# Kernel tuning notes

Measured on AMD Instinct MI355X. Metric: run time of the kernel, lower is better.

Reference implementation:

```python
import jax, jax.numpy as jnp
import numpy as np

B, D, L, K = 4096, 2048, 16384, 64  # batch, input_dim, latent_dim, topk


def setup_inputs() -> dict:
    key = jax.random.key(0)
    k_x, k_w = jax.random.split(key, 2)
    x = jax.random.normal(k_x, (B, D), dtype=jnp.float32)
    # torch init: randn(input_dim, latent_dim) / sqrt(input_dim)
    W_enc = jax.random.normal(k_w, (D, L), dtype=jnp.float32) / np.float32(np.sqrt(D))
    b_enc = jnp.zeros((L,), dtype=jnp.float32)
    b_dec = jnp.zeros((D,), dtype=jnp.float32)
    return {"x": x, "W_enc": W_enc, "b_enc": b_enc, "b_dec": b_dec, "k": K}


def reference(x, W_enc, b_enc, b_dec, k):
    # encode: [B, D] @ [D, L] + [L]
    z = x @ W_enc + b_enc
    # topk sparsify on |z| (do_abs_topk=True): scatter a 0/1 mask, multiply
    _, idx = jax.lax.top_k(jnp.abs(z), k)                      # idx: [B, k]
    rows = jnp.arange(z.shape[0])[:, None]                     # [B, 1]
    mask = jnp.zeros_like(z).at[rows, idx].set(1.0)            # [B, L]
    z_sparse = z * mask
    # decode with tied weights: [B, L] @ [L, D] + [D]
    recon = z_sparse @ W_enc.T + b_dec
    return recon, z_sparse
```

## Files before the change

kernel.cpp:

```cpp
#include <hip/hip_runtime.h>
#include <stdint.h>

#define NB 4096
#define DD 2048
#define LL 16384
#define KT 64
#define WCAP 24
#define TAU 1.2e-2f
#define T3 1e-4f

typedef unsigned short u16;
typedef __bf16 bf16x8 __attribute__((ext_vector_type(8)));
typedef float f32x4 __attribute__((ext_vector_type(4)));
typedef unsigned short u16x4 __attribute__((ext_vector_type(4)));
typedef unsigned short u16x8 __attribute__((ext_vector_type(8)));

__device__ __forceinline__ float bf2f(u16 b) {
  return __uint_as_float(((unsigned)b) << 16);
}
__device__ __forceinline__ u16 f2bf(float f) {
  unsigned u = __float_as_uint(f);
  unsigned r = u + 0x7fffu + ((u >> 16) & 1u);
  return (u16)(r >> 16);
}

__global__ __launch_bounds__(256) void prep_x(const float* __restrict__ X,
                                              u16* __restrict__ Xh) {
  int i = (blockIdx.x * 256 + threadIdx.x) * 4;
  float4 v = *(const float4*)(X + i);
  u16x4 h;
  h[0] = f2bf(v.x); h[1] = f2bf(v.y); h[2] = f2bf(v.z); h[3] = f2bf(v.w);
  *(u16x4*)(Xh + i) = h;
}

__global__ __launch_bounds__(256) void prep_w(const float* __restrict__ W,
                                              u16* __restrict__ Wh,
                                              u16* __restrict__ Wl,
                                              float* __restrict__ Wt) {
  __shared__ float tile[64][65];
  int l0 = blockIdx.x * 64, d0 = blockIdx.y * 64;
  int t = threadIdx.x;
  int lx = (t & 15) * 4;
  int dq = t >> 4;
#pragma unroll
  for (int p = 0; p < 4; ++p) {
    int d = dq + p * 16;
    float4 v = *(const float4*)(W + (size_t)(d0 + d) * LL + l0 + lx);
    tile[d][lx + 0] = v.x; tile[d][lx + 1] = v.y;
    tile[d][lx + 2] = v.z; tile[d][lx + 3] = v.w;
  }
  __syncthreads();
  int dx = (t & 15) * 4;
  int lq = t >> 4;
#pragma unroll
  for (int p = 0; p < 4; ++p) {
    int l = lq + p * 16;
    u16x4 h, lo;
    float4 wv;
#pragma unroll
    for (int q = 0; q < 4; ++q) {
      float w = tile[dx + q][l];
      u16 hb = f2bf(w);
      h[q] = hb;
      lo[q] = f2bf(w - bf2f(hb));
      ((float*)&wv)[q] = w;
    }
    size_t o = (size_t)(l0 + l) * DD + d0 + dx;
    *(u16x4*)(Wh + o) = h;
    *(u16x4*)(Wl + o) = lo;
    *(float4*)(Wt + o) = wv;
  }
}

#define TBM 256
#define TBN 256
#define TBK 64
#define NKT (DD / TBK)

__device__ __forceinline__ void async16(const u16* g, u16* l) {
  __builtin_amdgcn_global_load_lds(
      (const __attribute__((address_space(1))) unsigned int*)g,
      (__attribute__((address_space(3))) unsigned int*)l, 16, 0, 0);
}

#define STAGE(HF, TAU_)                                                      \
  do {                                                                       \
    const u16* g_ = ((HF) < 2 ? Abase : Bbase) +                             \
                    (size_t)(((HF)&1) * 128 + rr) * DD + ((TAU_) << 6) +     \
                    scol;                                                    \
    u16* l_ = ((HF) < 2 ? As : Bs) + ((TAU_)&1) * (TBM * TBK) +              \
              (((HF)&1) * 128) * TBK + t * 8;                                \
    async16(g_, l_);                                                         \
    async16(g_ + (size_t)64 * DD, l_ + 4096);                                \
  } while (0)

#define LDA(DST, DB, MQ)                                                     \
  do {                                                                       \
    const u16* p_ = As + (DB) * (TBM * TBK) + (wm + (MQ)*64 + fr) * TBK;     \
    _Pragma("unroll") for (int i_ = 0; i_ < 4; ++i_) {                       \
      DST[i_][0] = *(const bf16x8*)(p_ + i_ * (16 * TBK) + c0);              \
      DST[i_][1] = *(const bf16x8*)(p_ + i_ * (16 * TBK) + c1);              \
    }                                                                        \
  } while (0)

#define LDBQ(DB, NQ)                                                         \
  do {                                                                       \
    const u16* p_ = Bs + (DB) * (TBN * TBK) + (wn + (NQ)*32 + fr) * TBK;     \
    _Pragma("unroll") for (int j_ = 0; j_ < 2; ++j_) {                       \
      bq[j_][0] = *(const bf16x8*)(p_ + j_ * (16 * TBK) + c0);               \
      bq[j_][1] = *(const bf16x8*)(p_ + j_ * (16 * TBK) + c1);               \
    }                                                                        \
  } while (0)

#define MFMAQ_R(AF, MQ, NQ, IB, IE)                                          \
  do {                                                                       \
    _Pragma("unroll") for (int i_ = (IB); i_ < (IE); ++i_)                   \
        _Pragma("unroll") for (int j_ = 0; j_ < 2; ++j_) {                   \
      f32x4 a_ = acc[(MQ)*4 + i_][(NQ)*2 + j_];                              \
      a_ = __builtin_amdgcn_mfma_f32_16x16x32_bf16(AF[i_][0], bq[j_][0], a_, \
                                                   0, 0, 0);                 \
      a_ = __builtin_amdgcn_mfma_f32_16x16x32_bf16(AF[i_][1], bq[j_][1], a_, \
                                                   0, 0, 0);                 \
      acc[(MQ)*4 + i_][(NQ)*2 + j_] = a_;                                    \
    }                                                                        \
  } while (0)

#define MFMAQ(AF, MQ, NQ) MFMAQ_R(AF, MQ, NQ, 0, 4)

#define BAR __builtin_amdgcn_s_barrier()
#define LGKM0 asm volatile("s_waitcnt lgkmcnt(0)")
#define LGKM8 asm volatile("s_waitcnt lgkmcnt(8)")
#define LGKM12 asm volatile("s_waitcnt lgkmcnt(12)")
#define SCHED0 __builtin_amdgcn_sched_barrier(0)
#define PRIO1 __builtin_amdgcn_s_setprio(1)
#define PRIO0 __builtin_amdgcn_s_setprio(0)

__global__ __launch_bounds__(512, 2) void encode_gemm(
    const u16* __restrict__ Xh,
    const u16* __restrict__ Wh,
    const float* __restrict__ benc,
    float* __restrict__ Z) {
  __shared__ u16 As[2 * TBM * TBK];
  __shared__ u16 Bs[2 * TBN * TBK];
  int t = threadIdx.x;
  int m0 = blockIdx.y * TBM;
  int n0 = blockIdx.x * TBN;

  int lane = t & 63, w = t >> 6;
  int wm = (w & 1) * 128;
  int wn = (w >> 1) * 64;
  int fr = lane & 15;
  int fq = lane >> 4;
  int c0 = ((fq ^ (fr & 7)) << 3);
  int c1 = (((4 + fq) ^ (fr & 7)) << 3);
  int rr = t >> 3;
  int scol = (((t & 7) ^ (rr & 7)) << 3);

  const u16* Abase = Xh + (size_t)m0 * DD;
  const u16* Bbase = Wh + (size_t)n0 * DD;

  f32x4 acc[8][4] = {};
  bf16x8 af0[4][2], af1[4][2], bq[2][2];

  STAGE(0, 0); STAGE(1, 0); STAGE(2, 0); STAGE(3, 0);
  asm volatile("s_waitcnt vmcnt(4)" ::: "memory");
  STAGE(0, 1); STAGE(1, 1); STAGE(2, 1);
  asm volatile("s_waitcnt vmcnt(6)" ::: "memory");
  BAR;

  for (int it = 0; it < NKT / 2; ++it) {
    const int notlast = (it < NKT / 2 - 1);
    LDBQ(0, 0);
    LDA(af0, 0, 0);
    LDA(af1, 0, 1);
    STAGE(3, 2 * it + 1);
    LGKM12; PRIO1; MFMAQ_R(af0, 0, 0, 0, 2);
    LGKM8;  MFMAQ_R(af0, 0, 0, 2, 4);
    LGKM0;  MFMAQ(af1, 1, 0); PRIO0;
    LDBQ(0, 1);
    LGKM0; SCHED0; BAR;
    if (notlast) { STAGE(0, 2 * it + 2); STAGE(1, 2 * it + 2); STAGE(2, 2 * it + 2); }
    PRIO1; MFMAQ(af0, 0, 1); MFMAQ(af1, 1, 1); PRIO0;
    if (notlast) asm volatile("s_waitcnt vmcnt(6)" ::: "memory");
    else         asm volatile("s_waitcnt vmcnt(0)" ::: "memory");
    BAR;
    LDBQ(1, 0);
    LDA(af0, 1, 0);
    LDA(af1, 1, 1);
    if (notlast) STAGE(3, 2 * it + 2);
    LGKM12; PRIO1; MFMAQ_R(af0, 0, 0, 0, 2);
    LGKM8;  MFMAQ_R(af0, 0, 0, 2, 4);
    LGKM0;  MFMAQ(af1, 1, 0); PRIO0;
    LDBQ(1, 1);
    LGKM0; SCHED0; BAR;
    if (notlast) { STAGE(0, 2 * it + 3); STAGE(1, 2 * it + 3); STAGE(2, 2 * it + 3); }
    PRIO1; MFMAQ(af0, 0, 1); MFMAQ(af1, 1, 1); PRIO0;
    if (notlast) asm volatile("s_waitcnt vmcnt(6)" ::: "memory");
    BAR;
  }

  int rbase = m0 + wm + fq * 4;
#pragma unroll
  for (int nr = 0; nr < 4; ++nr) {
    int col = n0 + wn + nr * 16 + fr;
    float be = benc[col];
#pragma unroll
    for (int mr = 0; mr < 8; ++mr) {
      int row = rbase + mr * 16;
#pragma unroll
      for (int r = 0; r < 4; ++r)
        Z[(size_t)(row + r) * LL + col] = acc[mr][nr][r] + be;
    }
  }
}

__global__ __launch_bounds__(512) void topkfix_kernel(
    const float* __restrict__ Z, const float* __restrict__ X32,
    const float* __restrict__ benc, const u16* __restrict__ Wh,
    const u16* __restrict__ Wl, const float* __restrict__ Wt,
    float* __restrict__ ZS, int* __restrict__ TKI, float* __restrict__ TKV,
    int r0) {
  int lrow = blockIdx.x, grow = r0 + lrow, t = threadIdx.x;
  const float* zr = Z + (size_t)lrow * LL;
  float* zs = ZS + (size_t)lrow * LL;

  uint4 kv[8];
#pragma unroll
  for (int i = 0; i < 8; ++i) {
    float4 v = ((const float4*)zr)[t + i * 512];
    kv[i].x = __float_as_uint(v.x) & 0x7fffffffu;
    kv[i].y = __float_as_uint(v.y) & 0x7fffffffu;
    kv[i].z = __float_as_uint(v.z) & 0x7fffffffu;
    kv[i].w = __float_as_uint(v.w) & 0x7fffffffu;
  }
  float4 z4 = {0.f, 0.f, 0.f, 0.f};
#pragma unroll
  for (int i = 0; i < 8; ++i) ((float4*)zs)[t + i * 512] = z4;

  __shared__ int red[2][8];
  unsigned cut = 0;
  for (int bit = 30; bit >= 16; --bit) {
    int ph = bit & 1;
    unsigned ct = cut | (1u << bit);
    int cnt = 0;
#pragma unroll
    for (int i = 0; i < 8; ++i)
      cnt += (kv[i].x >= ct) + (kv[i].y >= ct) + (kv[i].z >= ct) + (kv[i].w >= ct);
    for (int off = 32; off > 0; off >>= 1) cnt += __shfl_down(cnt, off, 64);
    if ((t & 63) == 0) red[ph][t >> 6] = cnt;
    __syncthreads();
    int total = 0;
#pragma unroll
    for (int wv = 0; wv < 8; ++wv) total += red[ph][wv];
    if (total >= KT) cut = ct;
  }

  float c16 = __uint_as_float(cut);
  float cnx = __uint_as_float(cut + 0x10000u);
  float chi = cnx + TAU;
  float clo = c16 - TAU; if (clo < 0.f) clo = 0.f;
  unsigned hiKey = __float_as_uint(chi);
  unsigned loKey = (clo > 0.f) ? __float_as_uint(clo) : 0u;

  __shared__ unsigned nsel, ntie;
  __shared__ int widx[WCAP];
  if (t == 0) { nsel = 0; ntie = 0; }
  __syncthreads();

#pragma unroll
  for (int i = 0; i < 8; ++i) {
    int base = 4 * (t + i * 512);
    unsigned k4[4] = {kv[i].x, kv[i].y, kv[i].z, kv[i].w};
#pragma unroll
    for (int q = 0; q < 4; ++q) {
      unsigned key = k4[q];
      int idx = base + q;
      if (key > hiKey) {
        unsigned p = atomicAdd(&nsel, 1u);
        if (p < KT) {
          float v = zr[idx];
          TKI[grow * KT + p] = idx;
          TKV[grow * KT + p] = v;
          zs[idx] = v;
        }
      } else if (key >= loKey) {
        unsigned p = atomicAdd(&ntie, 1u);
        if (p < WCAP) widx[p] = idx;
      }
    }
  }
  __syncthreads();
  int ns = (int)nsel; if (ns > KT) ns = KT;
  if (t >= ns && t < KT) { TKI[grow * KT + t] = 0; TKV[grow * KT + t] = 0.f; }
  int wcnt = (int)ntie; if (wcnt > WCAP) wcnt = WCAP;
  int deferred = KT - ns;
  if (deferred <= 0) return;
  if (deferred > wcnt) deferred = wcnt;

  if (wcnt == deferred) {
    if (t < wcnt) {
      int idx = widx[t];
      float v = zr[idx];
      TKI[grow * KT + ns + t] = idx;
      TKV[grow * KT + ns + t] = v;
      zs[idx] = v;
    }
    return;
  }

  int wid = t >> 6, ln = t & 63;
  __shared__ float xs[DD];
  __shared__ double wz[WCAP];
  __shared__ int exact_flag[WCAP];
  for (int i = t; i < DD; i += 512) xs[i] = X32[(size_t)grow * DD + i];
  __syncthreads();
  for (int j = wid; j < wcnt; j += 8) {
    int idx = widx[j];
    const u16* wh = Wh + (size_t)idx * DD;
    const u16* wl = Wl + (size_t)idx * DD;
    double p = 0.0;
#pragma unroll
    for (int kb = 0; kb < 8; ++kb) {
      int k = kb * 256 + ln * 4;
      u16x4 h4 = *(const u16x4*)(wh + k);
      u16x4 l4 = *(const u16x4*)(wl + k);
      f32x4 x4 = *(const f32x4*)(xs + k);
#pragma unroll
      for (int e = 0; e < 4; ++e)
        p += (double)x4[e] * ((double)bf2f(h4[e]) + (double)bf2f(l4[e]));
    }
    for (int off = 32; off > 0; off >>= 1) p += __shfl_down(p, off, 64);
    if (ln == 0) wz[j] = p + (double)benc[idx];
  }
  __syncthreads();

  if (t == 0) {
    int taken = 0;
    double b = 0.0;
    for (int s = 0; s < deferred; ++s) {
      int best = -1; double bv = -1.0;
      for (int j = 0; j < wcnt; ++j) {
        if (taken & (1 << j)) continue;
        double a = fabs(wz[j]);
        if (best < 0 || a > bv || (a == bv && widx[j] < widx[best])) { best = j; bv = a; }
      }
      taken |= (1 << best);
      b = bv;
    }
    for (int j = 0; j < wcnt; ++j)
      exact_flag[j] = (fabs(fabs(wz[j]) - b) < (double)T3) ? 1 : 0;
  }
  __syncthreads();
  for (int j = wid; j < wcnt; j += 8) {
    if (!exact_flag[j]) continue;
    int idx = widx[j];
    const float* wrow = Wt + (size_t)idx * DD;
    double p = 0.0;
#pragma unroll 4
    for (int k = ln; k < DD; k += 64)
      p += (double)xs[k] * (double)wrow[k];
    for (int off = 32; off > 0; off >>= 1) p += __shfl_down(p, off, 64);
    if (ln == 0) wz[j] = p + (double)benc[idx];
  }
  __syncthreads();

  if (t == 0) {
    int taken = 0;
    for (int s = 0; s < deferred; ++s) {
      int best = -1; double bv = -1.0;
      for (int j = 0; j < wcnt; ++j) {
        if (taken & (1 << j)) continue;
        double a = fabs(wz[j]);
        if (best < 0 || a > bv || (a == bv && widx[j] < widx[best])) { best = j; bv = a; }
      }
      taken |= (1 << best);
      int idx = widx[best];
      float v = (float)wz[best];
      TKI[grow * KT + ns + s] = idx;
      TKV[grow * KT + ns + s] = v;
      zs[idx] = v;
    }
  }
}

__global__ __launch_bounds__(256) void decode_kernel(
    const u16* __restrict__ Wh, const float* __restrict__ bdec,
    const int* __restrict__ TKI, const float* __restrict__ TKV,
    float* __restrict__ OUT) {
  int row = blockIdx.x, t = threadIdx.x;
  __shared__ int sidx[KT];
  __shared__ float sval[KT];
  if (t < KT) {
    sidx[t] = TKI[row * KT + t] & (LL - 1);
    sval[t] = TKV[row * KT + t];
  }
  __syncthreads();
  int d0 = t * 8;
  float acc[8] = {0.f, 0.f, 0.f, 0.f, 0.f, 0.f, 0.f, 0.f};
#pragma unroll 8
  for (int j = 0; j < KT; ++j) {
    const u16x8 wv = *(const u16x8*)(Wh + (size_t)sidx[j] * DD + d0);
    float v = sval[j];
#pragma unroll
    for (int e = 0; e < 8; ++e) acc[e] = fmaf(v, bf2f(wv[e]), acc[e]);
  }
  float4 o0, o1;
  o0.x = acc[0] + bdec[d0 + 0]; o0.y = acc[1] + bdec[d0 + 1];
  o0.z = acc[2] + bdec[d0 + 2]; o0.w = acc[3] + bdec[d0 + 3];
  o1.x = acc[4] + bdec[d0 + 4]; o1.y = acc[5] + bdec[d0 + 5];
  o1.z = acc[6] + bdec[d0 + 6]; o1.w = acc[7] + bdec[d0 + 7];
  float* dst = OUT + (size_t)row * DD + d0;
  *(float4*)dst = o0;
  *(float4*)(dst + 4) = o1;
}

extern "C" void kernel_launch(void* const* d_in, const int* in_sizes, int n_in,
                              void* d_out, int out_size, void* d_ws,
                              size_t ws_size, hipStream_t stream) {
  const float* X = (const float*)d_in[0];
  const float* W = (const float*)d_in[1];
  const float* benc = (const float*)d_in[2];
  const float* bdec = (const float*)d_in[3];

  char* ws = (char*)d_ws;
  const size_t XH_B = (size_t)NB * DD * 2;
  const size_t WH_B = (size_t)LL * DD * 2;
  const size_t WT_B = (size_t)LL * DD * 4;
  const size_t TKI_B = (size_t)NB * KT * 4;
  u16* Xh = (u16*)ws;
  u16* Wh = (u16*)(ws + XH_B);
  u16* Wl = (u16*)(ws + XH_B + WH_B);
  float* Wt = (float*)(ws + XH_B + 2 * WH_B);
  int* TKI = (int*)(ws + XH_B + 2 * WH_B + WT_B);
  float* TKV = (float*)(ws + XH_B + 2 * WH_B + WT_B + TKI_B);
  float* Zc = (float*)(ws + XH_B + 2 * WH_B + WT_B + 2 * TKI_B);

  size_t fixed = XH_B + 2 * WH_B + WT_B + 2 * TKI_B;
  size_t avail = (ws_size > fixed) ? (ws_size - fixed) : 0;
  int chunk = (int)(avail / ((size_t)LL * 4));
  chunk = (chunk / TBM) * TBM;
  if (chunk > NB) chunk = NB;
  if (chunk < TBM) chunk = TBM;

  float* out_recon = (float*)d_out;
  float* out_zs = (float*)d_out + (size_t)NB * DD;

  prep_x<<<NB * DD / 1024, 256, 0, stream>>>(X, Xh);
  prep_w<<<dim3(LL / 64, DD / 64), 256, 0, stream>>>(W, Wh, Wl, Wt);
  for (int r0 = 0; r0 < NB; r0 += chunk) {
    int rows = NB - r0; if (rows > chunk) rows = chunk;
    encode_gemm<<<dim3(LL / TBN, rows / TBM), 512, 0, stream>>>(
        Xh + (size_t)r0 * DD, Wh, benc, Zc);
    topkfix_kernel<<<rows, 512, 0, stream>>>(
        Zc, X, benc, Wh, Wl, Wt, out_zs + (size_t)r0 * LL, TKI, TKV, r0);
  }
  decode_kernel<<<NB, 256, 0, stream>>>(Wh, bdec, TKI, TKV, out_recon);
}
```

Measured before the change: 1.159 ms.

## Drop split-bf16 weight copy, use single fp32 recheck, rework GEMM barrier schedule

Removes the hi/lo bf16 weight split and the two-pass refinement in the top-k fixup, so every boundary candidate is rescored once with fp32 weights and vectorized loads. The encode GEMM main loop is reordered with extra workgroup barriers around each MFMA quarter, and the global stage loads are spread between the compute phases. Decode unroll goes from 8 to 16. This writes one less weight array in prep and drops a fixup pass, but the added barriers may stall waves in the main GEMM.

```diff
diff --git a/kernel.cpp b/kernel.cpp
--- a/kernel.cpp
+++ b/kernel.cpp
@@ -7,7 +7,6 @@
 #define KT 64
 #define WCAP 24
 #define TAU 1.2e-2f
-#define T3 1e-4f
 
 typedef unsigned short u16;
 typedef __bf16 bf16x8 __attribute__((ext_vector_type(8)));
@@ -35,7 +34,6 @@
 
 __global__ __launch_bounds__(256) void prep_w(const float* __restrict__ W,
                                               u16* __restrict__ Wh,
-                                              u16* __restrict__ Wl,
                                               float* __restrict__ Wt) {
   __shared__ float tile[64][65];
   int l0 = blockIdx.x * 64, d0 = blockIdx.y * 64;
@@ -55,19 +53,16 @@
 #pragma unroll
   for (int p = 0; p < 4; ++p) {
     int l = lq + p * 16;
-    u16x4 h, lo;
+    u16x4 h;
     float4 wv;
 #pragma unroll
     for (int q = 0; q < 4; ++q) {
       float w = tile[dx + q][l];
-      u16 hb = f2bf(w);
-      h[q] = hb;
-      lo[q] = f2bf(w - bf2f(hb));
+      h[q] = f2bf(w);
       ((float*)&wv)[q] = w;
     }
     size_t o = (size_t)(l0 + l) * DD + d0 + dx;
     *(u16x4*)(Wh + o) = h;
-    *(u16x4*)(Wl + o) = lo;
     *(float4*)(Wt + o) = wv;
   }
 }
@@ -112,9 +107,9 @@
     }                                                                        \
   } while (0)
 
-#define MFMAQ_R(AF, MQ, NQ, IB, IE)                                          \
+#define MFMAQ(AF, MQ, NQ)                                                    \
   do {                                                                       \
-    _Pragma("unroll") for (int i_ = (IB); i_ < (IE); ++i_)                   \
+    _Pragma("unroll") for (int i_ = 0; i_ < 4; ++i_)                         \
         _Pragma("unroll") for (int j_ = 0; j_ < 2; ++j_) {                   \
       f32x4 a_ = acc[(MQ)*4 + i_][(NQ)*2 + j_];                              \
       a_ = __builtin_amdgcn_mfma_f32_16x16x32_bf16(AF[i_][0], bq[j_][0], a_, \
@@ -125,13 +120,9 @@
     }                                                                        \
   } while (0)
 
-#define MFMAQ(AF, MQ, NQ) MFMAQ_R(AF, MQ, NQ, 0, 4)
-
 #define BAR __builtin_amdgcn_s_barrier()
 #define LGKM0 asm volatile("s_waitcnt lgkmcnt(0)")
 #define LGKM8 asm volatile("s_waitcnt lgkmcnt(8)")
-#define LGKM12 asm volatile("s_waitcnt lgkmcnt(12)")
-#define SCHED0 __builtin_amdgcn_sched_barrier(0)
 #define PRIO1 __builtin_amdgcn_s_setprio(1)
 #define PRIO0 __builtin_amdgcn_s_setprio(0)
 
@@ -170,31 +161,33 @@
 
   for (int it = 0; it < NKT / 2; ++it) {
     const int notlast = (it < NKT / 2 - 1);
+    LDA(af0, 0, 0);
     LDBQ(0, 0);
-    LDA(af0, 0, 0);
     LDA(af1, 0, 1);
     STAGE(3, 2 * it + 1);
-    LGKM12; PRIO1; MFMAQ_R(af0, 0, 0, 0, 2);
-    LGKM8;  MFMAQ_R(af0, 0, 0, 2, 4);
-    LGKM0;  MFMAQ(af1, 1, 0); PRIO0;
+    BAR; LGKM8; PRIO1; MFMAQ(af0, 0, 0); PRIO0; BAR;
+    LGKM0; PRIO1; MFMAQ(af1, 1, 0); PRIO0;
     LDBQ(0, 1);
-    LGKM0; SCHED0; BAR;
-    if (notlast) { STAGE(0, 2 * it + 2); STAGE(1, 2 * it + 2); STAGE(2, 2 * it + 2); }
-    PRIO1; MFMAQ(af0, 0, 1); MFMAQ(af1, 1, 1); PRIO0;
+    BAR;
+    if (notlast) STAGE(0, 2 * it + 2);
+    BAR; LGKM0; PRIO1; MFMAQ(af0, 0, 1); PRIO0; BAR;
+    if (notlast) { STAGE(1, 2 * it + 2); STAGE(2, 2 * it + 2); }
+    BAR; PRIO1; MFMAQ(af1, 1, 1); PRIO0;
     if (notlast) asm volatile("s_waitcnt vmcnt(6)" ::: "memory");
     else         asm volatile("s_waitcnt vmcnt(0)" ::: "memory");
     BAR;
+    LDA(af0, 1, 0);
     LDBQ(1, 0);
-    LDA(af0, 1, 0);
     LDA(af1, 1, 1);
     if (notlast) STAGE(3, 2 * it + 2);
-    LGKM12; PRIO1; MFMAQ_R(af0, 0, 0, 0, 2);
-    LGKM8;  MFMAQ_R(af0, 0, 0, 2, 4);
-    LGKM0;  MFMAQ(af1, 1, 0); PRIO0;
+    BAR; LGKM8; PRIO1; MFMAQ(af0, 0, 0); PRIO0; BAR;
+    LGKM0; PRIO1; MFMAQ(af1, 1, 0); PRIO0;
     LDBQ(1, 1);
-    LGKM0; SCHED0; BAR;
-    if (notlast) { STAGE(0, 2 * it + 3); STAGE(1, 2 * it + 3); STAGE(2, 2 * it + 3); }
-    PRIO1; MFMAQ(af0, 0, 1); MFMAQ(af1, 1, 1); PRIO0;
+    BAR;
+    if (notlast) STAGE(0, 2 * it + 3);
+    BAR; LGKM0; PRIO1; MFMAQ(af0, 0, 1); PRIO0; BAR;
+    if (notlast) { STAGE(1, 2 * it + 3); STAGE(2, 2 * it + 3); }
+    BAR; PRIO1; MFMAQ(af1, 1, 1); PRIO0;
     if (notlast) asm volatile("s_waitcnt vmcnt(6)" ::: "memory");
     BAR;
   }
@@ -216,8 +209,7 @@
 
 __global__ __launch_bounds__(512) void topkfix_kernel(
     const float* __restrict__ Z, const float* __restrict__ X32,
-    const float* __restrict__ benc, const u16* __restrict__ Wh,
-    const u16* __restrict__ Wl, const float* __restrict__ Wt,
+    const float* __restrict__ benc, const float* __restrict__ Wt,
     float* __restrict__ ZS, int* __restrict__ TKI, float* __restrict__ TKV,
     int r0) {
   int lrow = blockIdx.x, grow = r0 + lrow, t = threadIdx.x;
@@ -311,54 +303,21 @@
   int wid = t >> 6, ln = t & 63;
   __shared__ float xs[DD];
   __shared__ double wz[WCAP];
-  __shared__ int exact_flag[WCAP];
   for (int i = t; i < DD; i += 512) xs[i] = X32[(size_t)grow * DD + i];
   __syncthreads();
   for (int j = wid; j < wcnt; j += 8) {
-    int idx = widx[j];
-    const u16* wh = Wh + (size_t)idx * DD;
-    const u16* wl = Wl + (size_t)idx * DD;
-    double p = 0.0;
-#pragma unroll
-    for (int kb = 0; kb < 8; ++kb) {
-      int k = kb * 256 + ln * 4;
-      u16x4 h4 = *(const u16x4*)(wh + k);
-      u16x4 l4 = *(const u16x4*)(wl + k);
-      f32x4 x4 = *(const f32x4*)(xs + k);
-#pragma unroll
-      for (int e = 0; e < 4; ++e)
-        p += (double)x4[e] * ((double)bf2f(h4[e]) + (double)bf2f(l4[e]));
-    }
-    for (int off = 32; off > 0; off >>= 1) p += __shfl_down(p, off, 64);
-    if (ln == 0) wz[j] = p + (double)benc[idx];
-  }
-  __syncthreads();
-
-  if (t == 0) {
-    int taken = 0;
-    double b = 0.0;
-    for (int s = 0; s < deferred; ++s) {
-      int best = -1; double bv = -1.0;
-      for (int j = 0; j < wcnt; ++j) {
-        if (taken & (1 << j)) continue;
-        double a = fabs(wz[j]);
-        if (best < 0 || a > bv || (a == bv && widx[j] < widx[best])) { best = j; bv = a; }
-      }
-      taken |= (1 << best);
-      b = bv;
-    }
-    for (int j = 0; j < wcnt; ++j)
-      exact_flag[j] = (fabs(fabs(wz[j]) - b) < (double)T3) ? 1 : 0;
-  }
-  __syncthreads();
-  for (int j = wid; j < wcnt; j += 8) {
-    if (!exact_flag[j]) continue;
     int idx = widx[j];
     const float* wrow = Wt + (size_t)idx * DD;
     double p = 0.0;
-#pragma unroll 4
-    for (int k = ln; k < DD; k += 64)
-      p += (double)xs[k] * (double)wrow[k];
+#pragma unroll
+    for (int kb = 0; kb < 8; ++kb) {
+      int k = kb * 256 + ln * 4;
+      f32x4 w4 = *(const f32x4*)(wrow + k);
+      f32x4 x4 = *(const f32x4*)(xs + k);
+#pragma unroll
+      for (int e = 0; e < 4; ++e)
+        p += (double)x4[e] * (double)w4[e];
+    }
     for (int off = 32; off > 0; off >>= 1) p += __shfl_down(p, off, 64);
     if (ln == 0) wz[j] = p + (double)benc[idx];
   }
@@ -397,7 +356,7 @@
   __syncthreads();
   int d0 = t * 8;
   float acc[8] = {0.f, 0.f, 0.f, 0.f, 0.f, 0.f, 0.f, 0.f};
-#pragma unroll 8
+#pragma unroll 16
   for (int j = 0; j < KT; ++j) {
     const u16x8 wv = *(const u16x8*)(Wh + (size_t)sidx[j] * DD + d0);
     float v = sval[j];
@@ -429,13 +388,12 @@
   const size_t TKI_B = (size_t)NB * KT * 4;
   u16* Xh = (u16*)ws;
   u16* Wh = (u16*)(ws + XH_B);
-  u16* Wl = (u16*)(ws + XH_B + WH_B);
-  float* Wt = (float*)(ws + XH_B + 2 * WH_B);
-  int* TKI = (int*)(ws + XH_B + 2 * WH_B + WT_B);
-  float* TKV = (float*)(ws + XH_B + 2 * WH_B + WT_B + TKI_B);
-  float* Zc = (float*)(ws + XH_B + 2 * WH_B + WT_B + 2 * TKI_B);
-
-  size_t fixed = XH_B + 2 * WH_B + WT_B + 2 * TKI_B;
+  float* Wt = (float*)(ws + XH_B + WH_B);
+  int* TKI = (int*)(ws + XH_B + WH_B + WT_B);
+  float* TKV = (float*)(ws + XH_B + WH_B + WT_B + TKI_B);
+  float* Zc = (float*)(ws + XH_B + WH_B + WT_B + 2 * TKI_B);
+
+  size_t fixed = XH_B + WH_B + WT_B + 2 * TKI_B;
   size_t avail = (ws_size > fixed) ? (ws_size - fixed) : 0;
   int chunk = (int)(avail / ((size_t)LL * 4));
   chunk = (chunk / TBM) * TBM;
@@ -446,13 +404,13 @@
   float* out_zs = (float*)d_out + (size_t)NB * DD;
 
   prep_x<<<NB * DD / 1024, 256, 0, stream>>>(X, Xh);
-  prep_w<<<dim3(LL / 64, DD / 64), 256, 0, stream>>>(W, Wh, Wl, Wt);
+  prep_w<<<dim3(LL / 64, DD / 64), 256, 0, stream>>>(W, Wh, Wt);
   for (int r0 = 0; r0 < NB; r0 += chunk) {
     int rows = NB - r0; if (rows > chunk) rows = chunk;
     encode_gemm<<<dim3(LL / TBN, rows / TBM), 512, 0, stream>>>(
         Xh + (size_t)r0 * DD, Wh, benc, Zc);
     topkfix_kernel<<<rows, 512, 0, stream>>>(
-        Zc, X, benc, Wh, Wl, Wt, out_zs + (size_t)r0 * LL, TKI, TKV, r0);
+        Zc, X, benc, Wt, out_zs + (size_t)r0 * LL, TKI, TKV, r0);
   }
   decode_kernel<<<NB, 256, 0, stream>>>(Wh, bdec, TKI, TKV, out_recon);
 }
```

After: 1.119 ms. 1.04x faster.
